# Optimization experiments

Hardware: AMD Instinct MI355X
Metric: run time of the kernel (lower is better)

The kernel has to match this reference:

```python
import jax, jax.numpy as jnp
import numpy as np

N_NODES = 50000
N_EDGES = 1600000
IN_DIM = 128
N_HEADS = 8
OUT_DIM = 16
LEAKY_SLOPE = 0.2


def setup_inputs() -> dict:
    key = jax.random.key(0)
    k1, k2, k3, k4, k5, k6 = jax.random.split(key, 6)
    x = jax.random.normal(k1, (N_NODES, IN_DIM), dtype=jnp.float32)
    W = jax.random.normal(k2, (N_HEADS * OUT_DIM, IN_DIM), dtype=jnp.float32) * (1.414 / np.sqrt(IN_DIM))
    attn_l = jax.random.normal(k3, (N_HEADS, OUT_DIM), dtype=jnp.float32) * 0.5
    attn_r = jax.random.normal(k4, (N_HEADS, OUT_DIM), dtype=jnp.float32) * 0.5
    src = jax.random.randint(k5, (N_EDGES,), 0, N_NODES, dtype=jnp.int64) if jax.config.jax_enable_x64 else jax.random.randint(k5, (N_EDGES,), 0, N_NODES, dtype=jnp.int32)
    dst = jax.random.randint(k6, (N_EDGES,), 0, N_NODES, dtype=src.dtype)
    return {"x": x, "W": W, "attn_l": attn_l, "attn_r": attn_r, "src": src, "dst": dst}


def reference(x, W, attn_l, attn_r, src, dst):
    n = x.shape[0]
    # fc projection -> [N, H, D]
    ft = (x @ W.T).reshape(n, N_HEADS, OUT_DIM)
    # per-node attention logits (bmm with [H,D,1] vector == contraction over D) -> [N, H]
    a1 = jnp.einsum('nhd,hd->nh', ft, attn_l)
    a2 = jnp.einsum('nhd,hd->nh', ft, attn_r)
    # per-edge score: leaky_relu(a1[src] + a2[dst]) -> [E, H]
    e = jax.nn.leaky_relu(a1[src] + a2[dst], negative_slope=LEAKY_SLOPE)
    # segment softmax over incoming edges of each dst node (numerically stable)
    seg_max = jax.ops.segment_max(e, dst, num_segments=n)          # [N, H]
    seg_max = jnp.where(jnp.isfinite(seg_max), seg_max, 0.0)       # isolated nodes -> 0
    e_exp = jnp.exp(e - seg_max[dst])                              # [E, H]
    denom = jax.ops.segment_sum(e_exp, dst, num_segments=n)        # [N, H]
    alpha = e_exp / denom[dst]                                     # [E, H]
    # weighted scatter-sum of src messages -> [N, H, D]
    msgs = ft[src] * alpha[:, :, None]                             # [E, H, D]
    out = jax.ops.segment_sum(msgs, dst, num_segments=n)
    return out
```

## Files before the change

### kernel.cpp

```cpp
#include <hip/hip_runtime.h>
#include <math.h>

#define N_NODES 50000
#define N_EDGES 1600000
#define IN_DIM 128
#define N_HEADS 8
#define OUT_DIM 16
#define HD 128
#define DEG_CAP 128
#define NBUCK 784
#define BCAP 2560
#define CHUNK 4096
#define BIN_BLOCKS ((N_EDGES + CHUNK - 1) / CHUNK)
#define PBLK ((N_NODES + 31) / 32)

__device__ __forceinline__ unsigned short f2bf(float f) {
    union { float f; unsigned int u; } v; v.f = f;
    unsigned int u = v.u;
    unsigned int r = (u + 0x7fffu + ((u >> 16) & 1u)) >> 16;
    return (unsigned short)r;
}

__device__ __forceinline__ void scan_nbuck_excl(int* arr, int* part) {
    int t = threadIdx.x;
    int v0 = 0, v1 = 0, v2 = 0, v3 = 0, cs = 0;
    if (t < NBUCK / 4) {
        v0 = arr[4 * t]; v1 = arr[4 * t + 1]; v2 = arr[4 * t + 2]; v3 = arr[4 * t + 3];
        cs = v0 + v1 + v2 + v3;
    }
    part[t] = cs;
    __syncthreads();
    for (int d = 1; d < 256; d <<= 1) {
        int u = (t >= d) ? part[t - d] : 0;
        __syncthreads();
        part[t] += u;
        __syncthreads();
    }
    if (t < NBUCK / 4) {
        int run = part[t] - cs;
        arr[4 * t] = run; run += v0;
        arr[4 * t + 1] = run; run += v1;
        arr[4 * t + 2] = run; run += v2;
        arr[4 * t + 3] = run;
    }
    __syncthreads();
}

__global__ void k_transpose_w(const float* __restrict__ W, float* __restrict__ Wt,
                              int* __restrict__ bucket_cnt, int* __restrict__ ovf_cnt) {
    int g = blockIdx.x * 256 + threadIdx.x;
    if (g < NBUCK) bucket_cnt[g] = 0;
    if (g == 0) *ovf_cnt = 0;
    if (g >= (HD * IN_DIM) / 4) return;
    int c  = g >> 5;
    int k4 = g & 31;
    float4 v = ((const float4*)W)[g];
    int k = k4 * 4;
    Wt[(k + 0) * HD + c] = v.x;
    Wt[(k + 1) * HD + c] = v.y;
    Wt[(k + 2) * HD + c] = v.z;
    Wt[(k + 3) * HD + c] = v.w;
}

__global__ __launch_bounds__(256, 2) void k_proj_bin(
    const float* __restrict__ x, const float* __restrict__ Wt,
    const float* __restrict__ attn_l, const float* __restrict__ attn_r,
    unsigned short* __restrict__ ftb, float* __restrict__ a1, float* __restrict__ a2,
    const int* __restrict__ src, const int* __restrict__ dst,
    unsigned int* __restrict__ region, int* __restrict__ bucket_cnt,
    int* __restrict__ ovf_cnt, unsigned int* __restrict__ ovf) {
    __shared__ __align__(16) char smem[23680];
    int tid = threadIdx.x;

    if (blockIdx.x < PBLK) {
        float (*red_l)[32] = (float(*)[32])smem;
        float (*red_r)[32] = (float(*)[32])(smem + 4096);

        int cb = (tid & 31) * 4;
        int nb = (tid >> 5) * 4;
        int node0 = blockIdx.x * 32;

        float4 acc[4];
        acc[0] = acc[1] = acc[2] = acc[3] = make_float4(0.f, 0.f, 0.f, 0.f);

        const float* xrow[4];
#pragma unroll
        for (int i = 0; i < 4; i++) {
            int n = node0 + nb + i;
            if (n >= N_NODES) n = N_NODES - 1;
            xrow[i] = x + (size_t)n * IN_DIM;
        }

#pragma unroll 2
        for (int k = 0; k < IN_DIM; k += 4) {
            float4 w0 = *(const float4*)(Wt + (k + 0) * HD + cb);
            float4 w1 = *(const float4*)(Wt + (k + 1) * HD + cb);
            float4 w2 = *(const float4*)(Wt + (k + 2) * HD + cb);
            float4 w3 = *(const float4*)(Wt + (k + 3) * HD + cb);
#pragma unroll
            for (int i = 0; i < 4; i++) {
                float4 xv = *(const float4*)(xrow[i] + k);
                acc[i].x = fmaf(xv.w, w3.x, fmaf(xv.z, w2.x, fmaf(xv.y, w1.x, fmaf(xv.x, w0.x, acc[i].x))));
                acc[i].y = fmaf(xv.w, w3.y, fmaf(xv.z, w2.y, fmaf(xv.y, w1.y, fmaf(xv.x, w0.y, acc[i].y))));
                acc[i].z = fmaf(xv.w, w3.z, fmaf(xv.z, w2.z, fmaf(xv.y, w1.z, fmaf(xv.x, w0.z, acc[i].z))));
                acc[i].w = fmaf(xv.w, w3.w, fmaf(xv.z, w2.w, fmaf(xv.y, w1.w, fmaf(xv.x, w0.w, acc[i].w))));
            }
        }

#pragma unroll
        for (int i = 0; i < 4; i++) {
            int n = node0 + nb + i;
            if (n < N_NODES) {
                ushort4 us;
                us.x = f2bf(acc[i].x); us.y = f2bf(acc[i].y);
                us.z = f2bf(acc[i].z); us.w = f2bf(acc[i].w);
                *(ushort4*)(ftb + (size_t)n * HD + cb) = us;
            }
        }

        int h   = cb >> 4;
        int sub = cb & 15;
        float4 al = *(const float4*)(attn_l + h * OUT_DIM + sub);
        float4 ar = *(const float4*)(attn_r + h * OUT_DIM + sub);
        int col = (h << 2) | (sub >> 2);
#pragma unroll
        for (int i = 0; i < 4; i++) {
            float pl = acc[i].x * al.x + acc[i].y * al.y + acc[i].z * al.z + acc[i].w * al.w;
            float pr = acc[i].x * ar.x + acc[i].y * ar.y + acc[i].z * ar.z + acc[i].w * ar.w;
            red_l[nb + i][col] = pl;
            red_r[nb + i][col] = pr;
        }
        __syncthreads();
        int nl = tid >> 3, hh = tid & 7;
        int n = node0 + nl;
        if (n < N_NODES) {
            float s1 = red_l[nl][hh * 4 + 0] + red_l[nl][hh * 4 + 1] + red_l[nl][hh * 4 + 2] + red_l[nl][hh * 4 + 3];
            float s2 = red_r[nl][hh * 4 + 0] + red_r[nl][hh * 4 + 1] + red_r[nl][hh * 4 + 2] + red_r[nl][hh * 4 + 3];
            a1[n * N_HEADS + hh] = s1;
            a2[n * N_HEADS + hh] = s2;
        }
    } else {
        unsigned int* stage = (unsigned int*)smem;
        int* hist  = (int*)(smem + 16384);
        int* delta = (int*)(smem + 19520);
        int* part  = (int*)(smem + 22656);

        int t = tid;
        int base = (blockIdx.x - PBLK) * CHUNK;
        int nvalid = min(CHUNK, N_EDGES - base);

        for (int i = t; i < NBUCK; i += 256) hist[i] = 0;
        __syncthreads();

        unsigned int mypack[CHUNK / 256];
#pragma unroll
        for (int k = 0; k < CHUNK / 256; k++) {
            int i = t + k * 256;
            if (i < nvalid) {
                int s = src[base + i];
                int d = dst[base + i];
                unsigned int p = ((unsigned int)d << 16) | (unsigned int)s;
                mypack[k] = p;
                atomicAdd(&hist[d >> 6], 1);
            }
        }
        __syncthreads();
        for (int i = t; i < NBUCK; i += 256) {
            int h = hist[i];
            delta[i] = (h > 0) ? atomicAdd(&bucket_cnt[i], h) : 0;
        }
        __syncthreads();
        scan_nbuck_excl(hist, part);
        for (int i = t; i < NBUCK; i += 256) delta[i] -= hist[i];
        __syncthreads();
#pragma unroll
        for (int k = 0; k < CHUNK / 256; k++) {
            int i = t + k * 256;
            if (i < nvalid) {
                unsigned int p = mypack[k];
                int slot = atomicAdd(&hist[p >> 22], 1);
                stage[slot] = p;
            }
        }
        __syncthreads();
        for (int i = t; i < nvalid; i += 256) {
            unsigned int p = stage[i];
            int b = p >> 22;
            int pos = delta[b] + i;
            if (pos < BCAP) region[(size_t)b * BCAP + pos] = p;
            else { int o = atomicAdd(ovf_cnt, 1); ovf[o] = p; }
        }
    }
}

__global__ __launch_bounds__(256) void k_place(
    const unsigned int* __restrict__ region, const int* __restrict__ bucket_cnt,
    const int* __restrict__ ovf_cnt, const unsigned int* __restrict__ ovf,
    int* __restrict__ offs, int* __restrict__ esrc) {
    int b = blockIdx.x;
    int t = threadIdx.x;
    __shared__ int sb[NBUCK], part[256];
    __shared__ int hist[64], sc[64], curs[64];

    for (int i = t; i < NBUCK; i += 256) sb[i] = bucket_cnt[i];
    if (t < 64) hist[t] = 0;
    __syncthreads();
    scan_nbuck_excl(sb, part);

    int truec = bucket_cnt[b];
    int base_b = sb[b];
    int rc = min(truec, BCAP);
    const unsigned int* reg = region + (size_t)b * BCAP;

    for (int i = t; i < rc; i += 256) atomicAdd(&hist[(reg[i] >> 16) & 63], 1);
    int no = 0;
    if (truec > BCAP) {
        no = *ovf_cnt;
        for (int i = t; i < no; i += 256)
            if ((int)(ovf[i] >> 22) == b) atomicAdd(&hist[(ovf[i] >> 16) & 63], 1);
    }
    __syncthreads();
    int h = (t < 64) ? hist[t] : 0;
    if (t < 64) sc[t] = h;
    __syncthreads();
    for (int d = 1; d < 64; d <<= 1) {
        int u = (t >= d && t < 64) ? sc[t - d] : 0;
        __syncthreads();
        if (t < 64) sc[t] += u;
        __syncthreads();
    }
    if (t < 64) {
        int pos0 = base_b + sc[t] - h;
        int node = b * 64 + t;
        if (node < N_NODES) offs[node] = pos0;
        curs[t] = pos0;
    }
    if (b == 0 && t == 0) offs[N_NODES] = N_EDGES;
    __syncthreads();
    for (int i = t; i < rc; i += 256) {
        unsigned int p = reg[i];
        int pos = atomicAdd(&curs[(p >> 16) & 63], 1);
        esrc[pos] = (int)(p & 0xffffu);
    }
    if (truec > BCAP) {
        for (int i = t; i < no; i += 256) {
            unsigned int p = ovf[i];
            if ((int)(p >> 22) == b) {
                int pos = atomicAdd(&curs[(p >> 16) & 63], 1);
                esrc[pos] = (int)(p & 0xffffu);
            }
        }
    }
}

__global__ __launch_bounds__(256) void k_aggregate(
    const unsigned short* __restrict__ ftb, const float* __restrict__ a1,
    const float* __restrict__ a2, const int* __restrict__ offs,
    const int* __restrict__ esrc, float* __restrict__ out) {
    __shared__ float lw[4][DEG_CAP * N_HEADS];
    __shared__ int   ls[4][DEG_CAP];

    int wid  = threadIdx.x >> 6;
    int lane = threadIdx.x & 63;
    int node = blockIdx.x * 4 + wid;
    float* w  = lw[wid];
    int*   si = ls[wid];

    int off = offs[node];
    int deg = offs[node + 1] - off;

    int h1 = lane & 7;
    int es = lane >> 3;
    float a2h = a2[node * N_HEADS + h1];

    float l = 0.f;
    for (int base = 0; base < deg; base += 8) {
        int e = base + es;
        if (e < deg) {
            int s = esrc[off + e];
            float t = a1[s * N_HEADS + h1] + a2h;
            t = t > 0.f ? t : 0.2f * t;
            float ww = __expf(t);
            l += ww;
            if (e < DEG_CAP) {
                w[e * N_HEADS + h1] = ww;
                if (h1 == 0) si[e] = s;
            }
        }
    }
    l += __shfl_xor(l, 8);
    l += __shfl_xor(l, 16);
    l += __shfl_xor(l, 32);
    float invl = (deg > 0) ? 1.f / l : 0.f;

    int lim = min(deg, DEG_CAP);
    for (int e = es; e < lim; e += 8) w[e * N_HEADS + h1] *= invl;

    int hl = lane >> 3;
    float invl2 = __shfl(invl, hl);
    float a2h2  = __shfl(a2h, hl);

    float accx = 0.f, accy = 0.f;
#pragma unroll 8
    for (int j = 0; j < lim; j++) {
        float ww = w[j * N_HEADS + hl];
        int s = si[j];
        unsigned int p = *(const unsigned int*)(ftb + (size_t)s * HD + lane * 2);
        float fx = __uint_as_float(p << 16);
        float fy = __uint_as_float(p & 0xffff0000u);
        accx = fmaf(ww, fx, accx);
        accy = fmaf(ww, fy, accy);
    }
    for (int j = DEG_CAP; j < deg; j++) {
        int s = esrc[off + j];
        float t = a1[s * N_HEADS + hl] + a2h2;
        t = t > 0.f ? t : 0.2f * t;
        float ww = __expf(t) * invl2;
        unsigned int p = *(const unsigned int*)(ftb + (size_t)s * HD + lane * 2);
        accx = fmaf(ww, __uint_as_float(p << 16), accx);
        accy = fmaf(ww, __uint_as_float(p & 0xffff0000u), accy);
    }

    float2 o; o.x = accx; o.y = accy;
    *(float2*)(out + (size_t)node * HD + lane * 2) = o;
}

extern "C" void kernel_launch(void* const* d_in, const int* in_sizes, int n_in,
                              void* d_out, int out_size, void* d_ws, size_t ws_size,
                              hipStream_t stream) {
    const float* x      = (const float*)d_in[0];
    const float* W      = (const float*)d_in[1];
    const float* attn_l = (const float*)d_in[2];
    const float* attn_r = (const float*)d_in[3];
    const int*   src    = (const int*)d_in[4];
    const int*   dst    = (const int*)d_in[5];
    float* out = (float*)d_out;

    char* ws = (char*)d_ws;
    size_t o = 0;
    auto alloc = [&](size_t bytes) -> char* {
        char* p = ws + o;
        o = (o + bytes + 255) & ~(size_t)255;
        return p;
    };
    unsigned short* ftb = (unsigned short*)alloc((size_t)N_NODES * HD * 2);
    float* a1          = (float*)alloc((size_t)N_NODES * N_HEADS * 4);
    float* a2          = (float*)alloc((size_t)N_NODES * N_HEADS * 4);
    float* Wt          = (float*)alloc((size_t)HD * IN_DIM * 4);
    unsigned int* region = (unsigned int*)alloc((size_t)NBUCK * BCAP * 4);
    int* bucket_cnt    = (int*)alloc((size_t)NBUCK * 4);
    int* ovf_cnt       = (int*)alloc(4);
    unsigned int* ovf  = (unsigned int*)alloc((size_t)N_EDGES * 4);
    int* offs          = (int*)alloc((size_t)(N_NODES + 1) * 4);
    int* esrc          = (int*)alloc((size_t)N_EDGES * 4);

    (void)in_sizes; (void)n_in; (void)out_size; (void)ws_size;

    k_transpose_w<<<16, 256, 0, stream>>>(W, Wt, bucket_cnt, ovf_cnt);
    k_proj_bin<<<PBLK + BIN_BLOCKS, 256, 0, stream>>>(
        x, Wt, attn_l, attn_r, ftb, a1, a2,
        src, dst, region, bucket_cnt, ovf_cnt, ovf);
    k_place<<<NBUCK, 256, 0, stream>>>(region, bucket_cnt, ovf_cnt, ovf, offs, esrc);
    k_aggregate<<<N_NODES / 4, 256, 0, stream>>>(ftb, a1, a2, offs, esrc, out);
}
```

Measured before the change: 229.4 us.

## Compute node projection with bf16 MFMA and shrink edge source indices to 16-bit

Replaces the scalar fp32 FMA projection with per-wavefront 16x16x32 bf16 MFMA tiles. Weights are pre-converted to bf16 in a prep kernel, and x is converted in registers. The per-tile output is staged through LDS to compute the a1/a2 attention logits and to write bf16 features coalesced. Sorted edge source indices are stored as 16-bit values, which halves that traffic, and the aggregation loop unroll goes from 8 to 16. The cost is bf16 rounding of x and W before the matmul, which lowers the precision of the logits; the 16-bit indices rely on the node count staying below 65536.

```diff
diff --git a/kernel.cpp b/kernel.cpp
--- a/kernel.cpp
+++ b/kernel.cpp
@@ -12,7 +12,12 @@
 #define BCAP 2560
 #define CHUNK 4096
 #define BIN_BLOCKS ((N_EDGES + CHUNK - 1) / CHUNK)
-#define PBLK ((N_NODES + 31) / 32)
+#define NTILE 3125
+#define PBLK ((NTILE + 3) / 4)
+#define TROW 132
+
+typedef __attribute__((ext_vector_type(8))) short bf16x8;
+typedef __attribute__((ext_vector_type(4))) float f32x4;
 
 __device__ __forceinline__ unsigned short f2bf(float f) {
     union { float f; unsigned int u; } v; v.f = f;
@@ -46,98 +51,100 @@
     __syncthreads();
 }
 
-__global__ void k_transpose_w(const float* __restrict__ W, float* __restrict__ Wt,
-                              int* __restrict__ bucket_cnt, int* __restrict__ ovf_cnt) {
+__global__ void k_prep(const float* __restrict__ W, unsigned short* __restrict__ Wb,
+                       int* __restrict__ bucket_cnt, int* __restrict__ ovf_cnt) {
     int g = blockIdx.x * 256 + threadIdx.x;
     if (g < NBUCK) bucket_cnt[g] = 0;
     if (g == 0) *ovf_cnt = 0;
     if (g >= (HD * IN_DIM) / 4) return;
-    int c  = g >> 5;
-    int k4 = g & 31;
     float4 v = ((const float4*)W)[g];
-    int k = k4 * 4;
-    Wt[(k + 0) * HD + c] = v.x;
-    Wt[(k + 1) * HD + c] = v.y;
-    Wt[(k + 2) * HD + c] = v.z;
-    Wt[(k + 3) * HD + c] = v.w;
-}
-
-__global__ __launch_bounds__(256, 2) void k_proj_bin(
-    const float* __restrict__ x, const float* __restrict__ Wt,
+    ushort4 us;
+    us.x = f2bf(v.x); us.y = f2bf(v.y); us.z = f2bf(v.z); us.w = f2bf(v.w);
+    ((ushort4*)Wb)[g] = us;
+}
+
+__global__ __launch_bounds__(256) void k_proj_bin(
+    const float* __restrict__ x, const unsigned short* __restrict__ Wb,
     const float* __restrict__ attn_l, const float* __restrict__ attn_r,
     unsigned short* __restrict__ ftb, float* __restrict__ a1, float* __restrict__ a2,
     const int* __restrict__ src, const int* __restrict__ dst,
     unsigned int* __restrict__ region, int* __restrict__ bucket_cnt,
     int* __restrict__ ovf_cnt, unsigned int* __restrict__ ovf) {
-    __shared__ __align__(16) char smem[23680];
+    __shared__ __align__(16) char smem[4 * 16 * TROW * 4];
     int tid = threadIdx.x;
 
     if (blockIdx.x < PBLK) {
-        float (*red_l)[32] = (float(*)[32])smem;
-        float (*red_r)[32] = (float(*)[32])(smem + 4096);
-
-        int cb = (tid & 31) * 4;
-        int nb = (tid >> 5) * 4;
-        int node0 = blockIdx.x * 32;
-
-        float4 acc[4];
-        acc[0] = acc[1] = acc[2] = acc[3] = make_float4(0.f, 0.f, 0.f, 0.f);
-
-        const float* xrow[4];
-#pragma unroll
-        for (int i = 0; i < 4; i++) {
-            int n = node0 + nb + i;
-            if (n >= N_NODES) n = N_NODES - 1;
-            xrow[i] = x + (size_t)n * IN_DIM;
-        }
-
-#pragma unroll 2
-        for (int k = 0; k < IN_DIM; k += 4) {
-            float4 w0 = *(const float4*)(Wt + (k + 0) * HD + cb);
-            float4 w1 = *(const float4*)(Wt + (k + 1) * HD + cb);
-            float4 w2 = *(const float4*)(Wt + (k + 2) * HD + cb);
-            float4 w3 = *(const float4*)(Wt + (k + 3) * HD + cb);
-#pragma unroll
-            for (int i = 0; i < 4; i++) {
-                float4 xv = *(const float4*)(xrow[i] + k);
-                acc[i].x = fmaf(xv.w, w3.x, fmaf(xv.z, w2.x, fmaf(xv.y, w1.x, fmaf(xv.x, w0.x, acc[i].x))));
-                acc[i].y = fmaf(xv.w, w3.y, fmaf(xv.z, w2.y, fmaf(xv.y, w1.y, fmaf(xv.x, w0.y, acc[i].y))));
-                acc[i].z = fmaf(xv.w, w3.z, fmaf(xv.z, w2.z, fmaf(xv.y, w1.z, fmaf(xv.x, w0.z, acc[i].z))));
-                acc[i].w = fmaf(xv.w, w3.w, fmaf(xv.z, w2.w, fmaf(xv.y, w1.w, fmaf(xv.x, w0.w, acc[i].w))));
-            }
-        }
-
-#pragma unroll
-        for (int i = 0; i < 4; i++) {
-            int n = node0 + nb + i;
-            if (n < N_NODES) {
-                ushort4 us;
-                us.x = f2bf(acc[i].x); us.y = f2bf(acc[i].y);
-                us.z = f2bf(acc[i].z); us.w = f2bf(acc[i].w);
-                *(ushort4*)(ftb + (size_t)n * HD + cb) = us;
-            }
-        }
-
-        int h   = cb >> 4;
-        int sub = cb & 15;
-        float4 al = *(const float4*)(attn_l + h * OUT_DIM + sub);
-        float4 ar = *(const float4*)(attn_r + h * OUT_DIM + sub);
-        int col = (h << 2) | (sub >> 2);
-#pragma unroll
-        for (int i = 0; i < 4; i++) {
-            float pl = acc[i].x * al.x + acc[i].y * al.y + acc[i].z * al.z + acc[i].w * al.w;
-            float pr = acc[i].x * ar.x + acc[i].y * ar.y + acc[i].z * ar.z + acc[i].w * ar.w;
-            red_l[nb + i][col] = pl;
-            red_r[nb + i][col] = pr;
-        }
-        __syncthreads();
-        int nl = tid >> 3, hh = tid & 7;
-        int n = node0 + nl;
-        if (n < N_NODES) {
-            float s1 = red_l[nl][hh * 4 + 0] + red_l[nl][hh * 4 + 1] + red_l[nl][hh * 4 + 2] + red_l[nl][hh * 4 + 3];
-            float s2 = red_r[nl][hh * 4 + 0] + red_r[nl][hh * 4 + 1] + red_r[nl][hh * 4 + 2] + red_r[nl][hh * 4 + 3];
-            a1[n * N_HEADS + hh] = s1;
-            a2[n * N_HEADS + hh] = s2;
+        int wid  = tid >> 6;
+        int tile = blockIdx.x * 4 + wid;
+        if (tile >= NTILE) return;
+        int lane = tid & 63;
+        int m = lane & 15, q = lane >> 4;
+        int node0 = tile * 16;
+
+        const float* xr = x + (size_t)(node0 + m) * IN_DIM + q * 8;
+        float4 xa[4][2];
+#pragma unroll
+        for (int ks = 0; ks < 4; ks++) {
+            xa[ks][0] = *(const float4*)(xr + ks * 32);
+            xa[ks][1] = *(const float4*)(xr + ks * 32 + 4);
+        }
+        bf16x8 afr[4];
+#pragma unroll
+        for (int ks = 0; ks < 4; ks++) {
+            afr[ks][0] = (short)f2bf(xa[ks][0].x); afr[ks][1] = (short)f2bf(xa[ks][0].y);
+            afr[ks][2] = (short)f2bf(xa[ks][0].z); afr[ks][3] = (short)f2bf(xa[ks][0].w);
+            afr[ks][4] = (short)f2bf(xa[ks][1].x); afr[ks][5] = (short)f2bf(xa[ks][1].y);
+            afr[ks][6] = (short)f2bf(xa[ks][1].z); afr[ks][7] = (short)f2bf(xa[ks][1].w);
+        }
+
+        float* tl = (float*)smem + wid * (16 * TROW);
+
+#pragma unroll
+        for (int h = 0; h < N_HEADS; h++) {
+            const unsigned short* wrow = Wb + (size_t)(h * 16 + m) * IN_DIM + q * 8;
+            f32x4 c = {0.f, 0.f, 0.f, 0.f};
+#pragma unroll
+            for (int ks = 0; ks < 4; ks++) {
+                bf16x8 bfr = *(const bf16x8*)(wrow + ks * 32);
+                c = __builtin_amdgcn_mfma_f32_16x16x32_bf16(afr[ks], bfr, c, 0, 0, 0);
+            }
+#pragma unroll
+            for (int r = 0; r < 4; r++)
+                tl[(q * 4 + r) * TROW + h * 16 + m] = c[r];
+        }
+
+        int nd = lane & 15;
+#pragma unroll
+        for (int hi = 0; hi < 2; hi++) {
+            int hh = (lane >> 4) + hi * 4;
+            const float4* rowv = (const float4*)(tl + nd * TROW + hh * 16);
+            const float4* alv  = (const float4*)(attn_l + hh * OUT_DIM);
+            const float4* arv  = (const float4*)(attn_r + hh * OUT_DIM);
+            float sl = 0.f, sr = 0.f;
+#pragma unroll
+            for (int d4 = 0; d4 < 4; d4++) {
+                float4 fv = rowv[d4];
+                float4 al = alv[d4];
+                float4 ar = arv[d4];
+                sl += fv.x * al.x + fv.y * al.y + fv.z * al.z + fv.w * al.w;
+                sr += fv.x * ar.x + fv.y * ar.y + fv.z * ar.z + fv.w * ar.w;
+            }
+            a1[(node0 + nd) * N_HEADS + hh] = sl;
+            a2[(node0 + nd) * N_HEADS + hh] = sr;
+        }
+
+#pragma unroll
+        for (int p = 0; p < 4; p++) {
+            int r = p * 4 + q;
+            const float* srcp = tl + r * TROW + m * 8;
+            float4 f0 = *(const float4*)(srcp);
+            float4 f1 = *(const float4*)(srcp + 4);
+            ushort4 u0, u1;
+            u0.x = f2bf(f0.x); u0.y = f2bf(f0.y); u0.z = f2bf(f0.z); u0.w = f2bf(f0.w);
+            u1.x = f2bf(f1.x); u1.y = f2bf(f1.y); u1.z = f2bf(f1.z); u1.w = f2bf(f1.w);
+            ushort4* dstp = (ushort4*)(ftb + (size_t)(node0 + r) * HD + m * 8);
+            dstp[0] = u0;
+            dstp[1] = u1;
         }
     } else {
         unsigned int* stage = (unsigned int*)smem;
@@ -196,7 +203,7 @@
 __global__ __launch_bounds__(256) void k_place(
     const unsigned int* __restrict__ region, const int* __restrict__ bucket_cnt,
     const int* __restrict__ ovf_cnt, const unsigned int* __restrict__ ovf,
-    int* __restrict__ offs, int* __restrict__ esrc) {
+    int* __restrict__ offs, unsigned short* __restrict__ esrc) {
     int b = blockIdx.x;
     int t = threadIdx.x;
     __shared__ int sb[NBUCK], part[256];
@@ -240,14 +247,14 @@
     for (int i = t; i < rc; i += 256) {
         unsigned int p = reg[i];
         int pos = atomicAdd(&curs[(p >> 16) & 63], 1);
-        esrc[pos] = (int)(p & 0xffffu);
+        esrc[pos] = (unsigned short)(p & 0xffffu);
     }
     if (truec > BCAP) {
         for (int i = t; i < no; i += 256) {
             unsigned int p = ovf[i];
             if ((int)(p >> 22) == b) {
                 int pos = atomicAdd(&curs[(p >> 16) & 63], 1);
-                esrc[pos] = (int)(p & 0xffffu);
+                esrc[pos] = (unsigned short)(p & 0xffffu);
             }
         }
     }
@@ -256,7 +263,7 @@
 __global__ __launch_bounds__(256) void k_aggregate(
     const unsigned short* __restrict__ ftb, const float* __restrict__ a1,
     const float* __restrict__ a2, const int* __restrict__ offs,
-    const int* __restrict__ esrc, float* __restrict__ out) {
+    const unsigned short* __restrict__ esrc, float* __restrict__ out) {
     __shared__ float lw[4][DEG_CAP * N_HEADS];
     __shared__ int   ls[4][DEG_CAP];
 
@@ -301,7 +308,7 @@
     float a2h2  = __shfl(a2h, hl);
 
     float accx = 0.f, accy = 0.f;
-#pragma unroll 8
+#pragma unroll 16
     for (int j = 0; j < lim; j++) {
         float ww = w[j * N_HEADS + hl];
         int s = si[j];
@@ -343,22 +350,22 @@
         o = (o + bytes + 255) & ~(size_t)255;
         return p;
     };
-    unsigned short* ftb = (unsigned short*)alloc((size_t)N_NODES * HD * 2);
-    float* a1          = (float*)alloc((size_t)N_NODES * N_HEADS * 4);
-    float* a2          = (float*)alloc((size_t)N_NODES * N_HEADS * 4);
-    float* Wt          = (float*)alloc((size_t)HD * IN_DIM * 4);
+    unsigned short* ftb  = (unsigned short*)alloc((size_t)N_NODES * HD * 2);
+    float* a1            = (float*)alloc((size_t)N_NODES * N_HEADS * 4);
+    float* a2            = (float*)alloc((size_t)N_NODES * N_HEADS * 4);
+    unsigned short* Wb   = (unsigned short*)alloc((size_t)HD * IN_DIM * 2);
     unsigned int* region = (unsigned int*)alloc((size_t)NBUCK * BCAP * 4);
-    int* bucket_cnt    = (int*)alloc((size_t)NBUCK * 4);
-    int* ovf_cnt       = (int*)alloc(4);
-    unsigned int* ovf  = (unsigned int*)alloc((size_t)N_EDGES * 4);
-    int* offs          = (int*)alloc((size_t)(N_NODES + 1) * 4);
-    int* esrc          = (int*)alloc((size_t)N_EDGES * 4);
+    int* bucket_cnt      = (int*)alloc((size_t)NBUCK * 4);
+    int* ovf_cnt         = (int*)alloc(4);
+    unsigned int* ovf    = (unsigned int*)alloc((size_t)N_EDGES * 4);
+    int* offs            = (int*)alloc((size_t)(N_NODES + 1) * 4);
+    unsigned short* esrc = (unsigned short*)alloc((size_t)N_EDGES * 2);
 
     (void)in_sizes; (void)n_in; (void)out_size; (void)ws_size;
 
-    k_transpose_w<<<16, 256, 0, stream>>>(W, Wt, bucket_cnt, ovf_cnt);
+    k_prep<<<16, 256, 0, stream>>>(W, Wb, bucket_cnt, ovf_cnt);
     k_proj_bin<<<PBLK + BIN_BLOCKS, 256, 0, stream>>>(
-        x, Wt, attn_l, attn_r, ftb, a1, a2,
+        x, Wb, attn_l, attn_r, ftb, a1, a2,
         src, dst, region, bucket_cnt, ovf_cnt, ovf);
     k_place<<<NBUCK, 256, 0, stream>>>(region, bucket_cnt, ovf_cnt, ovf, offs, esrc);
     k_aggregate<<<N_NODES / 4, 256, 0, stream>>>(ftb, a1, a2, offs, esrc, out);
```

Result: faster. 209.0 us (-8.9%).
